# Optimization experiments

Hardware: AMD Instinct MI355X
Metric: run time of the kernel (lower is better)

Reference implementation:

```python
import jax, jax.numpy as jnp
import numpy as np

N_NODES = 100000
N_EDGES = 1600000
DIM = 128
N_LAYERS = 3   # num_gc_layers
N_RES = 3      # residual VQ layers
N_CODE = 16    # codebook_size
N_GRAPHS = 512
BN_EPS = 1e-5
COMMIT_W = 0.25


def _l2norm(v):
    return v * jax.lax.rsqrt(jnp.sum(v * v, axis=-1, keepdims=True) + 1e-12)


def setup_inputs() -> dict:
    key = jax.random.key(0)
    ks = jax.random.split(key, 8)
    s = 0.05
    x = jax.random.normal(ks[0], (N_NODES, DIM), jnp.float32)
    edge_index = jax.random.randint(ks[1], (2, N_EDGES), 0, N_NODES)
    batch = jnp.sort(jax.random.randint(ks[2], (N_NODES,), 0, N_GRAPHS))
    W1 = jax.random.normal(ks[3], (N_LAYERS, DIM, DIM), jnp.float32) * s
    b1 = jnp.zeros((N_LAYERS, DIM), jnp.float32)
    W2 = jax.random.normal(ks[4], (N_LAYERS, DIM, DIM), jnp.float32) * s
    b2 = jnp.zeros((N_LAYERS, DIM), jnp.float32)
    gamma = jnp.ones((N_LAYERS, DIM), jnp.float32)
    beta = jnp.zeros((N_LAYERS, DIM), jnp.float32)
    codebooks = jax.random.normal(ks[5], (N_LAYERS, N_RES, N_CODE, DIM), jnp.float32)
    return dict(x=x, edge_index=edge_index, batch=batch, W1=W1, b1=b1,
                W2=W2, b2=b2, gamma=gamma, beta=beta, codebooks=codebooks)


def reference(x, edge_index, batch, W1, b1, W2, b2, gamma, beta, codebooks):
    src, dst = edge_index[0], edge_index[1]
    h = x
    xs, ids = [], []
    commit_loss = jnp.float32(0.0)
    for i in range(N_LAYERS):
        # GINConv, eps=0: MLP((1+eps)*x + sum_{j->i} x_j)
        agg = jax.ops.segment_sum(h[src], dst, num_segments=N_NODES)
        h = agg + h
        h = jax.nn.relu(h @ W1[i] + b1[i]) @ W2[i] + b2[i]  # Linear-ReLU-Linear
        h = jax.nn.relu(h)                                   # outer F.relu
        # BatchNorm1d (training-mode batch stats, biased variance)
        mean = jnp.mean(h, axis=0)
        var = jnp.var(h, axis=0)
        h = (h - mean) * jax.lax.rsqrt(var + BN_EPS) * gamma[i] + beta[i]
        xs.append(h)
        # Residual VQ with cosine-sim codebook (3 residual layers)
        r = h
        lids = []
        for l in range(N_RES):
            cbn = _l2norm(codebooks[i, l])           # [K, D] normalized codebook
            sim = _l2norm(r) @ cbn.T                  # [N, K] cosine similarity
            idx = jnp.argmax(sim, axis=-1)            # nearest code
            q = cbn[idx]                              # quantized residual
            commit_loss = commit_loss + COMMIT_W * jnp.mean(
                (jax.lax.stop_gradient(q) - r) ** 2)
            r = r - jax.lax.stop_gradient(q)
            lids.append(idx)
        ids.append(jnp.stack(lids, axis=1))           # [N, N_RES]
    xs_cat = jnp.concatenate(xs, axis=1)              # [N, DIM*N_LAYERS]
    xpool = jax.ops.segment_sum(xs_cat, batch, num_segments=N_GRAPHS)
    id_cat = jnp.concatenate(ids, axis=1)             # [N, N_RES*N_LAYERS]
    return xpool, xs_cat, commit_loss, id_cat
```

## Files before the change

### kernel.cpp

```cpp
#include <hip/hip_runtime.h>
#include <hip/hip_bf16.h>

#define N_NODES 100000
#define N_EDGES 1600000
#define DIM 128
#define NLAY 3
#define NRES 3
#define NCODE 16
#define NGRAPH 512
#define SCAN_NB ((N_NODES + 255) / 256)
#define GEMM_NB ((N_NODES + 63) / 64)

using bf16 = __hip_bfloat16;

__device__ inline void atomAddD(double* p, double v) { unsafeAtomicAdd(p, v); }

__device__ inline double ldx(const void* p, long i, int isbf) {
  if (isbf) return (double)__bfloat162float(((const bf16*)p)[i]);
  return (double)((const float*)p)[i];
}
__device__ inline void stout(void* p, long i, double v, int isbf) {
  if (isbf) ((bf16*)p)[i] = __float2bfloat16((float)v);
  else ((float*)p)[i] = (float)v;
}

__global__ void k_detect(const unsigned int* __restrict__ x, int* __restrict__ flag) {
  int tid = threadIdx.x;
  int cnt = 0;
  for (int j = tid; j < 1024; j += 256) {
    unsigned int u = x[j];
    int e = (u >> 7) & 0xFF;
    cnt += (e >= 100 && e <= 135) ? 1 : 0;
  }
  __shared__ int sh[256];
  sh[tid] = cnt; __syncthreads();
  for (int s = 128; s; s >>= 1) { if (tid < s) sh[tid] += sh[tid + s]; __syncthreads(); }
  if (tid == 0) flag[0] = (sh[0] > 512) ? 1 : 0;
}

__global__ __launch_bounds__(256) void k_convert_f(const void* __restrict__ x, float* __restrict__ hf,
                                                   long n, const int* __restrict__ flag) {
  int isbf = flag[0];
  long i = (long)blockIdx.x * 256 + threadIdx.x;
  if (i < n) hf[i] = (float)ldx(x, i, isbf);
}

__global__ __launch_bounds__(256) void k_hist(const int* __restrict__ ei, int* __restrict__ deg) {
  int e = blockIdx.x * 256 + threadIdx.x;
  if (e < N_EDGES) atomicAdd(&deg[ei[N_EDGES + e]], 1);
}

__global__ __launch_bounds__(256) void k_scan1(const int* __restrict__ deg, int* __restrict__ bsum) {
  int i = blockIdx.x * 256 + threadIdx.x;
  int v = (i < N_NODES) ? deg[i] : 0;
  for (int o = 32; o; o >>= 1) v += __shfl_xor(v, o);
  __shared__ int sh[4];
  if ((threadIdx.x & 63) == 0) sh[threadIdx.x >> 6] = v;
  __syncthreads();
  if (threadIdx.x == 0) bsum[blockIdx.x] = sh[0] + sh[1] + sh[2] + sh[3];
}

__global__ void k_scan2(int* __restrict__ bsum) {
  __shared__ int sh[512];
  int t = threadIdx.x;
  int v = (t < SCAN_NB) ? bsum[t] : 0;
  sh[t] = v; __syncthreads();
  for (int s = 1; s < 512; s <<= 1) {
    int add = (t >= s) ? sh[t - s] : 0;
    __syncthreads();
    sh[t] += add;
    __syncthreads();
  }
  if (t < SCAN_NB) bsum[t] = sh[t] - v;
}

__global__ __launch_bounds__(256) void k_scan3(const int* __restrict__ deg, const int* __restrict__ bsum,
                                               int* __restrict__ ofs, int* __restrict__ cursor) {
  int t = threadIdx.x;
  int i = blockIdx.x * 256 + t;
  int v = (i < N_NODES) ? deg[i] : 0;
  __shared__ int sh[256];
  sh[t] = v; __syncthreads();
  for (int s = 1; s < 256; s <<= 1) {
    int add = (t >= s) ? sh[t - s] : 0;
    __syncthreads();
    sh[t] += add;
    __syncthreads();
  }
  int excl = sh[t] - v + bsum[blockIdx.x];
  if (i < N_NODES) { ofs[i] = excl; cursor[i] = excl; }
  if (i == N_NODES - 1) ofs[N_NODES] = excl + v;
}

__global__ __launch_bounds__(256) void k_fill(const int* __restrict__ ei, int* __restrict__ cursor,
                                              int* __restrict__ csr) {
  int e = blockIdx.x * 256 + threadIdx.x;
  if (e < N_EDGES) {
    int d = ei[N_EDGES + e];
    int p = atomicAdd(&cursor[d], 1);
    csr[p] = ei[e];
  }
}

__global__ void k_cbn(const void* __restrict__ cb, double* __restrict__ cbn, const int* __restrict__ flag) {
  int isbf = flag[0];
  int b = blockIdx.x, d = threadIdx.x;
  double v0 = ldx(cb, (long)b * DIM + d, isbf);
  double v1 = ldx(cb, (long)b * DIM + d + 64, isbf);
  double ss = v0 * v0 + v1 * v1;
  for (int o = 32; o; o >>= 1) ss += __shfl_xor(ss, o);
  double inv = 1.0 / sqrt(ss + 1e-12);
  cbn[b * DIM + d] = v0 * inv;
  cbn[b * DIM + d + 64] = v1 * inv;
}

__global__ void k_gram(const double* __restrict__ cbn, double* __restrict__ G) {
  int b = blockIdx.x, t = threadIdx.x;
  int l = b / (48 * 48); int rem = b % (48 * 48); int a = rem / 48, c = rem % 48;
  const double* ra = cbn + (long)(l * 48 + a) * DIM;
  const double* rc = cbn + (long)(l * 48 + c) * DIM;
  double s = ra[t] * rc[t] + ra[t + 64] * rc[t + 64];
  for (int o = 32; o; o >>= 1) s += __shfl_xor(s, o);
  if (t == 0) G[b] = s;
}

__global__ __launch_bounds__(256) void k_gathgemm1(const float* __restrict__ hf,
                                                   const int* __restrict__ ofs,
                                                   const int* __restrict__ csr,
                                                   const float* __restrict__ W,
                                                   const float* __restrict__ bias,
                                                   float* __restrict__ out) {
  __shared__ float ul[64 * DIM];
  int tid = threadIdx.x;
  long base = (long)blockIdx.x * 64;
  int wave = tid >> 6, lane = tid & 63;
  for (int i = 0; i < 16; i++) {
    int row = wave * 16 + i;
    long node = base + row;
    double accx = 0.0, accy = 0.0;
    if (node < N_NODES) {
      int beg = ofs[node], end = ofs[node + 1];
      float2 sv = *(const float2*)&hf[node * DIM + lane * 2];
      accx = (double)sv.x; accy = (double)sv.y;
      int j = beg;
      for (; j + 7 < end; j += 8) {
        int s0 = csr[j], s1 = csr[j + 1], s2 = csr[j + 2], s3 = csr[j + 3];
        int s4 = csr[j + 4], s5 = csr[j + 5], s6 = csr[j + 6], s7 = csr[j + 7];
        float2 v0 = *(const float2*)&hf[(long)s0 * DIM + lane * 2];
        float2 v1 = *(const float2*)&hf[(long)s1 * DIM + lane * 2];
        float2 v2 = *(const float2*)&hf[(long)s2 * DIM + lane * 2];
        float2 v3 = *(const float2*)&hf[(long)s3 * DIM + lane * 2];
        float2 v4 = *(const float2*)&hf[(long)s4 * DIM + lane * 2];
        float2 v5 = *(const float2*)&hf[(long)s5 * DIM + lane * 2];
        float2 v6 = *(const float2*)&hf[(long)s6 * DIM + lane * 2];
        float2 v7 = *(const float2*)&hf[(long)s7 * DIM + lane * 2];
        accx += (double)v0.x; accy += (double)v0.y;
        accx += (double)v1.x; accy += (double)v1.y;
        accx += (double)v2.x; accy += (double)v2.y;
        accx += (double)v3.x; accy += (double)v3.y;
        accx += (double)v4.x; accy += (double)v4.y;
        accx += (double)v5.x; accy += (double)v5.y;
        accx += (double)v6.x; accy += (double)v6.y;
        accx += (double)v7.x; accy += (double)v7.y;
      }
      for (; j < end; j++) {
        int s0 = csr[j];
        float2 v0 = *(const float2*)&hf[(long)s0 * DIM + lane * 2];
        accx += (double)v0.x; accy += (double)v0.y;
      }
    }
    *(float2*)&ul[row * DIM + lane * 2] = make_float2((float)accx, (float)accy);
  }
  __syncthreads();
  int cl = tid & 31;
  int rw = tid >> 5;
  int c0 = cl * 4;
  float acc[8][4] = {};
  for (int k = 0; k < DIM; k += 4) {
    float4 w0 = *(const float4*)&W[(k + 0) * DIM + c0];
    float4 w1 = *(const float4*)&W[(k + 1) * DIM + c0];
    float4 w2 = *(const float4*)&W[(k + 2) * DIM + c0];
    float4 w3 = *(const float4*)&W[(k + 3) * DIM + c0];
#pragma unroll
    for (int r = 0; r < 8; r++) {
      float4 u = *(const float4*)&ul[(rw * 8 + r) * DIM + k];
      acc[r][0] += u.x * w0.x + u.y * w1.x + u.z * w2.x + u.w * w3.x;
      acc[r][1] += u.x * w0.y + u.y * w1.y + u.z * w2.y + u.w * w3.y;
      acc[r][2] += u.x * w0.z + u.y * w1.z + u.z * w2.z + u.w * w3.z;
      acc[r][3] += u.x * w0.w + u.y * w1.w + u.z * w2.w + u.w * w3.w;
    }
  }
  float4 bv = *(const float4*)&bias[c0];
#pragma unroll
  for (int r = 0; r < 8; r++) {
    long row = base + rw * 8 + r;
    if (row < N_NODES) {
      float4 o;
      o.x = fmaxf(acc[r][0] + bv.x, 0.f);
      o.y = fmaxf(acc[r][1] + bv.y, 0.f);
      o.z = fmaxf(acc[r][2] + bv.z, 0.f);
      o.w = fmaxf(acc[r][3] + bv.w, 0.f);
      *(float4*)&out[row * DIM + c0] = o;
    }
  }
}

__global__ __launch_bounds__(256) void k_gemm_relu_f(const float* __restrict__ in,
                                                     const float* __restrict__ W,
                                                     const float* __restrict__ bias,
                                                     float* __restrict__ out) {
  __shared__ float ul[64 * DIM];
  int tid = threadIdx.x;
  long base = (long)blockIdx.x * 64;
  for (int j = tid; j < 64 * DIM / 4; j += 256) {
    long row = base + (j >> 5);
    float4 v = make_float4(0.f, 0.f, 0.f, 0.f);
    if (row < N_NODES) v = *(const float4*)&in[base * DIM + (long)j * 4];
    *(float4*)&ul[j * 4] = v;
  }
  __syncthreads();
  int cl = tid & 31;
  int rw = tid >> 5;
  int c0 = cl * 4;
  float acc[8][4] = {};
  for (int k = 0; k < DIM; k += 4) {
    float4 w0 = *(const float4*)&W[(k + 0) * DIM + c0];
    float4 w1 = *(const float4*)&W[(k + 1) * DIM + c0];
    float4 w2 = *(const float4*)&W[(k + 2) * DIM + c0];
    float4 w3 = *(const float4*)&W[(k + 3) * DIM + c0];
#pragma unroll
    for (int r = 0; r < 8; r++) {
      float4 u = *(const float4*)&ul[(rw * 8 + r) * DIM + k];
      acc[r][0] += u.x * w0.x + u.y * w1.x + u.z * w2.x + u.w * w3.x;
      acc[r][1] += u.x * w0.y + u.y * w1.y + u.z * w2.y + u.w * w3.y;
      acc[r][2] += u.x * w0.z + u.y * w1.z + u.z * w2.z + u.w * w3.z;
      acc[r][3] += u.x * w0.w + u.y * w1.w + u.z * w2.w + u.w * w3.w;
    }
  }
  float4 bv = *(const float4*)&bias[c0];
#pragma unroll
  for (int r = 0; r < 8; r++) {
    long row = base + rw * 8 + r;
    if (row < N_NODES) {
      float4 o;
      o.x = fmaxf(acc[r][0] + bv.x, 0.f);
      o.y = fmaxf(acc[r][1] + bv.y, 0.f);
      o.z = fmaxf(acc[r][2] + bv.z, 0.f);
      o.w = fmaxf(acc[r][3] + bv.w, 0.f);
      *(float4*)&out[row * DIM + c0] = o;
    }
  }
}

__global__ __launch_bounds__(256) void k_bn_stats(const float* __restrict__ h, double* __restrict__ stats) {
  int tid = threadIdx.x; int col = tid & 127; int half = tid >> 7;
  double s = 0.0, s2 = 0.0;
  for (long r = blockIdx.x * 2 + half; r < N_NODES; r += 2048) {
    double v = (double)h[r * DIM + col];
    s += v; s2 += v * v;
  }
  __shared__ double ls[256], ls2[256];
  ls[tid] = s; ls2[tid] = s2;
  __syncthreads();
  if (tid < 128) {
    atomAddD(&stats[col], ls[tid] + ls[tid + 128]);
    atomAddD(&stats[DIM + col], ls2[tid] + ls2[tid + 128]);
  }
}

__global__ void k_bn_prep(const double* __restrict__ stats, const void* __restrict__ gamma,
                          const void* __restrict__ beta, double* __restrict__ ss,
                          int l, const int* __restrict__ flag) {
  int isbf = flag[0];
  int d = threadIdx.x;
  double mean = stats[d] / (double)N_NODES;
  double var = stats[DIM + d] / (double)N_NODES - mean * mean;
  double sc = ldx(gamma, (long)l * DIM + d, isbf) / sqrt(var + 1e-5);
  ss[d] = sc;
  ss[DIM + d] = ldx(beta, (long)l * DIM + d, isbf) - mean * sc;
}

__global__ __launch_bounds__(256) void k_post(float* __restrict__ h,
                                              const double* __restrict__ ss,
                                              const int* __restrict__ batch,
                                              void* __restrict__ out,
                                              double* __restrict__ xpool,
                                              double* __restrict__ hh,
                                              int l, const int* __restrict__ flag) {
  __shared__ float hl[64 * 132];
  __shared__ double hq[64 * 4];
  __shared__ int sbat[64];
  int isbf = flag[0];
  int tid = threadIdx.x;
  long base = (long)blockIdx.x * 64;
  if (tid < 64) {
    long row = base + tid;
    sbat[tid] = (row < N_NODES) ? batch[row] : -1;
  }
  int d = tid & 127, half = tid >> 7;
  double sc = ss[d], sh = ss[DIM + d];
  const long XS_BASE = (long)NGRAPH * DIM * NLAY;
  for (int rr = half; rr < 64; rr += 2) {
    long row = base + rr;
    float vf = 0.f;
    if (row < N_NODES) {
      double v = (double)h[row * DIM + d] * sc + sh;
      vf = (float)v;
      h[row * DIM + d] = vf;
      stout(out, XS_BASE + row * (DIM * NLAY) + l * DIM + d, v, isbf);
    }
    hl[rr * 132 + d] = vf;
  }
  __syncthreads();
  {
    int row = tid >> 2, q = tid & 3;
    double s2 = 0.0;
    const float* hp = &hl[row * 132 + q * 32];
#pragma unroll
    for (int i = 0; i < 32; i++) { double v = (double)hp[i]; s2 += v * v; }
    hq[row * 4 + q] = s2;
  }
  __syncthreads();
  if (tid < 64) {
    long n = base + tid;
    if (n < N_NODES) hh[n] = hq[tid * 4] + hq[tid * 4 + 1] + hq[tid * 4 + 2] + hq[tid * 4 + 3];
  } else if (tid >= 128) {
    int dd = tid - 128;
    int g = sbat[0];
    double acc = 0.0;
    for (int r = 0; r < 64; r++) {
      int gg = sbat[r];
      if (gg < 0) break;
      if (gg != g) {
        atomAddD(&xpool[(long)g * (DIM * NLAY) + l * DIM + dd], acc);
        acc = 0.0; g = gg;
      }
      acc += (double)hl[r * 132 + dd];
    }
    atomAddD(&xpool[(long)g * (DIM * NLAY) + l * DIM + dd], acc);
  }
}

__global__ __launch_bounds__(256) void k_dotH(const float* __restrict__ hn,
                                              const double* __restrict__ cbnL,
                                              float* __restrict__ dH) {
  __shared__ double cl[48 * 134];
  int tid = threadIdx.x;
  for (int j = tid; j < 48 * DIM; j += 256) { int c = j >> 7, k = j & 127; cl[c * 134 + k] = cbnL[j]; }
  __syncthreads();
  int ct = tid & 7; int c0 = ct * 6; int rt = tid >> 3;
  long r0 = (long)blockIdx.x * 64 + rt; long r1 = r0 + 32;
  long r0c = r0 < N_NODES ? r0 : (N_NODES - 1);
  long r1c = r1 < N_NODES ? r1 : (N_NODES - 1);
  double acc0[6] = {}, acc1[6] = {};
  for (int k = 0; k < DIM; k += 4) {
    float4 h0 = *(const float4*)&hn[r0c * DIM + k];
    float4 h1 = *(const float4*)&hn[r1c * DIM + k];
#pragma unroll
    for (int j = 0; j < 6; j++) {
      double2 ca = *(const double2*)&cl[(c0 + j) * 134 + k];
      double2 cb = *(const double2*)&cl[(c0 + j) * 134 + k + 2];
      acc0[j] += (double)h0.x * ca.x + (double)h0.y * ca.y + (double)h0.z * cb.x + (double)h0.w * cb.y;
      acc1[j] += (double)h1.x * ca.x + (double)h1.y * ca.y + (double)h1.z * cb.x + (double)h1.w * cb.y;
    }
  }
  if (r0 < N_NODES) {
#pragma unroll
    for (int j = 0; j < 6; j++) dH[r0 * 48 + c0 + j] = (float)acc0[j];
  }
  if (r1 < N_NODES) {
#pragma unroll
    for (int j = 0; j < 6; j++) dH[r1 * 48 + c0 + j] = (float)acc1[j];
  }
}

__global__ __launch_bounds__(256) void k_vq(const float* __restrict__ dH, const double* __restrict__ hh,
                                            const double* __restrict__ G, void* __restrict__ out,
                                            double* __restrict__ commit, int l, const int* __restrict__ flag) {
  int isbf = flag[0];
  __shared__ double Gl[48 * 48];
  int tid = threadIdx.x;
  for (int j = tid; j < 48 * 48; j += 256) Gl[j] = G[j];
  __syncthreads();
  long n = (long)blockIdx.x * 256 + tid;
  double csum = 0.0;
  if (n < N_NODES) {
    double dh[48];
#pragma unroll
    for (int c = 0; c < 48; c++) dh[c] = (double)dH[n * 48 + c];
    int i0 = 0; double b0 = dh[0];
#pragma unroll
    for (int c = 1; c < 16; c++) { if (dh[c] > b0) { b0 = dh[c]; i0 = c; } }
    int i1 = 0; double b1 = dh[16] - Gl[i0 * 48 + 16];
#pragma unroll
    for (int c = 1; c < 16; c++) {
      double s = dh[16 + c] - Gl[i0 * 48 + 16 + c];
      if (s > b1) { b1 = s; i1 = c; }
    }
    int i2 = 0; double b2 = dh[32] - Gl[i0 * 48 + 32] - Gl[(16 + i1) * 48 + 32];
#pragma unroll
    for (int c = 1; c < 16; c++) {
      double s = dh[32 + c] - Gl[i0 * 48 + 32 + c] - Gl[(16 + i1) * 48 + 32 + c];
      if (s > b2) { b2 = s; i2 = c; }
    }
    double r1s = hh[n] - 2.0 * b0 + Gl[i0 * 48 + i0];
    double r2s = r1s - 2.0 * b1 + Gl[(16 + i1) * 48 + 16 + i1];
    double r3s = r2s - 2.0 * b2 + Gl[(32 + i2) * 48 + 32 + i2];
    csum = r1s + r2s + r3s;
    const long IDS_BASE = (long)NGRAPH * DIM * NLAY + (long)N_NODES * DIM * NLAY + 1;
    long base = IDS_BASE + n * (NLAY * NRES) + l * NRES;
    stout(out, base + 0, (double)i0, isbf);
    stout(out, base + 1, (double)i1, isbf);
    stout(out, base + 2, (double)i2, isbf);
  }
  for (int o = 32; o; o >>= 1) csum += __shfl_xor(csum, o);
  if ((tid & 63) == 0 && csum != 0.0) atomAddD(commit, csum);
}

__global__ __launch_bounds__(256) void k_out(const double* __restrict__ xpool, const double* __restrict__ commit,
                                             void* __restrict__ out, const int* __restrict__ flag) {
  int isbf = flag[0];
  long i = (long)blockIdx.x * 256 + threadIdx.x;
  const long NP = (long)NGRAPH * DIM * NLAY;
  if (i < NP) {
    stout(out, i, xpool[i], isbf);
  } else if (i == NP) {
    double c = commit[0] * (0.25 / ((double)N_NODES * (double)DIM));
    stout(out, NP + (long)N_NODES * DIM * NLAY, c, isbf);
  }
}

extern "C" void kernel_launch(void* const* d_in, const int* in_sizes, int n_in,
                              void* d_out, int out_size, void* d_ws, size_t ws_size,
                              hipStream_t stream) {
  const void* x = d_in[0];
  const int* ei = (const int*)d_in[1];
  const int* batch = (const int*)d_in[2];
  const void* W1 = d_in[3];
  const void* b1 = d_in[4];
  const void* W2 = d_in[5];
  const void* b2 = d_in[6];
  const void* gamma = d_in[7];
  const void* beta = d_in[8];
  const void* cb = d_in[9];

  double* w = (double*)d_ws;
  double* cbn = w;
  double* G = cbn + 18432;
  double* stats = G + 6912;
  double* ss = stats + 256;
  double* hh = ss + 256;
  double* xpool = hh + N_NODES;
  double* commit = xpool + (long)NGRAPH * DIM * NLAY;
  float* W1f = (float*)(commit + 2);
  float* W2f = W1f + 49152;
  float* b1f = W2f + 49152;
  float* b2f = b1f + 384;
  float* H  = b2f + 384;
  float* T1 = H + 12800000;
  float* T2 = T1 + 12800000;
  float* dH = T2 + 12800000;
  int* ibuf = (int*)(dH + 4800000);
  int* flag = ibuf;
  int* deg = ibuf + 64;
  int* ofs = deg + N_NODES;
  int* cursor = ofs + N_NODES + 1;
  int* csr = cursor + N_NODES;
  int* bsum = csr + N_EDGES;

  k_detect<<<1, 256, 0, stream>>>((const unsigned int*)x, flag);
  hipMemsetAsync(xpool, 0, ((long)NGRAPH * DIM * NLAY + 1) * sizeof(double), stream);
  hipMemsetAsync(deg, 0, N_NODES * sizeof(int), stream);
  k_convert_f<<<50000, 256, 0, stream>>>(x, H, (long)N_NODES * DIM, flag);
  k_convert_f<<<192, 256, 0, stream>>>(W1, W1f, 49152, flag);
  k_convert_f<<<192, 256, 0, stream>>>(W2, W2f, 49152, flag);
  k_convert_f<<<2, 256, 0, stream>>>(b1, b1f, 384, flag);
  k_convert_f<<<2, 256, 0, stream>>>(b2, b2f, 384, flag);
  k_cbn<<<NLAY * NRES * NCODE, 64, 0, stream>>>(cb, cbn, flag);
  k_gram<<<NLAY * 48 * 48, 64, 0, stream>>>(cbn, G);
  k_hist<<<(N_EDGES + 255) / 256, 256, 0, stream>>>(ei, deg);
  k_scan1<<<SCAN_NB, 256, 0, stream>>>(deg, bsum);
  k_scan2<<<1, 512, 0, stream>>>(bsum);
  k_scan3<<<SCAN_NB, 256, 0, stream>>>(deg, bsum, ofs, cursor);
  k_fill<<<(N_EDGES + 255) / 256, 256, 0, stream>>>(ei, cursor, csr);

  for (int l = 0; l < NLAY; l++) {
    k_gathgemm1<<<GEMM_NB, 256, 0, stream>>>(H, ofs, csr, W1f + l * DIM * DIM, b1f + l * DIM, T2);
    k_gemm_relu_f<<<GEMM_NB, 256, 0, stream>>>(T2, W2f + l * DIM * DIM, b2f + l * DIM, T1);
    hipMemsetAsync(stats, 0, 256 * sizeof(double), stream);
    k_bn_stats<<<1024, 256, 0, stream>>>(T1, stats);
    k_bn_prep<<<1, 128, 0, stream>>>(stats, gamma, beta, ss, l, flag);
    k_post<<<GEMM_NB, 256, 0, stream>>>(T1, ss, batch, d_out, xpool, hh, l, flag);
    k_dotH<<<1563, 256, 0, stream>>>(T1, cbn + (long)l * 48 * DIM, dH);
    k_vq<<<391, 256, 0, stream>>>(dH, hh, G + l * 48 * 48, d_out, commit, l, flag);
    float* t = H; H = T1; T1 = t;
  }
  k_out<<<769, 256, 0, stream>>>(xpool, commit, d_out, flag);
}
```

Measured before the change: 1.711 ms.

## Split gather from GEMM, fuse BN stats into second GEMM and prep into post

The fused gather+GEMM kernel is split into a standalone gather kernel that runs one wave per node across many more blocks, followed by the plain GEMM. This raises parallelism for the latency-bound irregular gather. Batch-norm column sums are now accumulated in the epilogue of the second GEMM, with atomics spread over 8 slabs to reduce contention. The separate stats pass over T1 and the bn_prep launch are removed, and k_post derives scale and shift itself. In exchange the aggregated features take an extra round trip through global memory.

```diff
diff --git a/kernel.cpp b/kernel.cpp
--- a/kernel.cpp
+++ b/kernel.cpp
@@ -102,6 +102,35 @@
   }
 }
 
+__global__ __launch_bounds__(256) void k_gather(const float* __restrict__ hf,
+                                                const int* __restrict__ ofs,
+                                                const int* __restrict__ csr,
+                                                float* __restrict__ outQ) {
+  int node = blockIdx.x * 4 + (threadIdx.x >> 6);
+  int lane = threadIdx.x & 63;
+  int beg = ofs[node], end = ofs[node + 1];
+  float2 sv = *(const float2*)&hf[(long)node * DIM + lane * 2];
+  double accx = (double)sv.x, accy = (double)sv.y;
+  int j = beg;
+  for (; j + 3 < end; j += 4) {
+    int s0 = csr[j], s1 = csr[j + 1], s2 = csr[j + 2], s3 = csr[j + 3];
+    float2 v0 = *(const float2*)&hf[(long)s0 * DIM + lane * 2];
+    float2 v1 = *(const float2*)&hf[(long)s1 * DIM + lane * 2];
+    float2 v2 = *(const float2*)&hf[(long)s2 * DIM + lane * 2];
+    float2 v3 = *(const float2*)&hf[(long)s3 * DIM + lane * 2];
+    accx += (double)v0.x; accy += (double)v0.y;
+    accx += (double)v1.x; accy += (double)v1.y;
+    accx += (double)v2.x; accy += (double)v2.y;
+    accx += (double)v3.x; accy += (double)v3.y;
+  }
+  for (; j < end; j++) {
+    int s0 = csr[j];
+    float2 v0 = *(const float2*)&hf[(long)s0 * DIM + lane * 2];
+    accx += (double)v0.x; accy += (double)v0.y;
+  }
+  *(float2*)&outQ[(long)node * DIM + lane * 2] = make_float2((float)accx, (float)accy);
+}
+
 __global__ void k_cbn(const void* __restrict__ cb, double* __restrict__ cbn, const int* __restrict__ flag) {
   int isbf = flag[0];
   int b = blockIdx.x, d = threadIdx.x;
@@ -122,87 +151,6 @@
   double s = ra[t] * rc[t] + ra[t + 64] * rc[t + 64];
   for (int o = 32; o; o >>= 1) s += __shfl_xor(s, o);
   if (t == 0) G[b] = s;
-}
-
-__global__ __launch_bounds__(256) void k_gathgemm1(const float* __restrict__ hf,
-                                                   const int* __restrict__ ofs,
-                                                   const int* __restrict__ csr,
-                                                   const float* __restrict__ W,
-                                                   const float* __restrict__ bias,
-                                                   float* __restrict__ out) {
-  __shared__ float ul[64 * DIM];
-  int tid = threadIdx.x;
-  long base = (long)blockIdx.x * 64;
-  int wave = tid >> 6, lane = tid & 63;
-  for (int i = 0; i < 16; i++) {
-    int row = wave * 16 + i;
-    long node = base + row;
-    double accx = 0.0, accy = 0.0;
-    if (node < N_NODES) {
-      int beg = ofs[node], end = ofs[node + 1];
-      float2 sv = *(const float2*)&hf[node * DIM + lane * 2];
-      accx = (double)sv.x; accy = (double)sv.y;
-      int j = beg;
-      for (; j + 7 < end; j += 8) {
-        int s0 = csr[j], s1 = csr[j + 1], s2 = csr[j + 2], s3 = csr[j + 3];
-        int s4 = csr[j + 4], s5 = csr[j + 5], s6 = csr[j + 6], s7 = csr[j + 7];
-        float2 v0 = *(const float2*)&hf[(long)s0 * DIM + lane * 2];
-        float2 v1 = *(const float2*)&hf[(long)s1 * DIM + lane * 2];
-        float2 v2 = *(const float2*)&hf[(long)s2 * DIM + lane * 2];
-        float2 v3 = *(const float2*)&hf[(long)s3 * DIM + lane * 2];
-        float2 v4 = *(const float2*)&hf[(long)s4 * DIM + lane * 2];
-        float2 v5 = *(const float2*)&hf[(long)s5 * DIM + lane * 2];
-        float2 v6 = *(const float2*)&hf[(long)s6 * DIM + lane * 2];
-        float2 v7 = *(const float2*)&hf[(long)s7 * DIM + lane * 2];
-        accx += (double)v0.x; accy += (double)v0.y;
-        accx += (double)v1.x; accy += (double)v1.y;
-        accx += (double)v2.x; accy += (double)v2.y;
-        accx += (double)v3.x; accy += (double)v3.y;
-        accx += (double)v4.x; accy += (double)v4.y;
-        accx += (double)v5.x; accy += (double)v5.y;
-        accx += (double)v6.x; accy += (double)v6.y;
-        accx += (double)v7.x; accy += (double)v7.y;
-      }
-      for (; j < end; j++) {
-        int s0 = csr[j];
-        float2 v0 = *(const float2*)&hf[(long)s0 * DIM + lane * 2];
-        accx += (double)v0.x; accy += (double)v0.y;
-      }
-    }
-    *(float2*)&ul[row * DIM + lane * 2] = make_float2((float)accx, (float)accy);
-  }
-  __syncthreads();
-  int cl = tid & 31;
-  int rw = tid >> 5;
-  int c0 = cl * 4;
-  float acc[8][4] = {};
-  for (int k = 0; k < DIM; k += 4) {
-    float4 w0 = *(const float4*)&W[(k + 0) * DIM + c0];
-    float4 w1 = *(const float4*)&W[(k + 1) * DIM + c0];
-    float4 w2 = *(const float4*)&W[(k + 2) * DIM + c0];
-    float4 w3 = *(const float4*)&W[(k + 3) * DIM + c0];
-#pragma unroll
-    for (int r = 0; r < 8; r++) {
-      float4 u = *(const float4*)&ul[(rw * 8 + r) * DIM + k];
-      acc[r][0] += u.x * w0.x + u.y * w1.x + u.z * w2.x + u.w * w3.x;
-      acc[r][1] += u.x * w0.y + u.y * w1.y + u.z * w2.y + u.w * w3.y;
-      acc[r][2] += u.x * w0.z + u.y * w1.z + u.z * w2.z + u.w * w3.z;
-      acc[r][3] += u.x * w0.w + u.y * w1.w + u.z * w2.w + u.w * w3.w;
-    }
-  }
-  float4 bv = *(const float4*)&bias[c0];
-#pragma unroll
-  for (int r = 0; r < 8; r++) {
-    long row = base + rw * 8 + r;
-    if (row < N_NODES) {
-      float4 o;
-      o.x = fmaxf(acc[r][0] + bv.x, 0.f);
-      o.y = fmaxf(acc[r][1] + bv.y, 0.f);
-      o.z = fmaxf(acc[r][2] + bv.z, 0.f);
-      o.w = fmaxf(acc[r][3] + bv.w, 0.f);
-      *(float4*)&out[row * DIM + c0] = o;
-    }
-  }
 }
 
 __global__ __launch_bounds__(256) void k_gemm_relu_f(const float* __restrict__ in,
@@ -252,36 +200,80 @@
   }
 }
 
-__global__ __launch_bounds__(256) void k_bn_stats(const float* __restrict__ h, double* __restrict__ stats) {
-  int tid = threadIdx.x; int col = tid & 127; int half = tid >> 7;
-  double s = 0.0, s2 = 0.0;
-  for (long r = blockIdx.x * 2 + half; r < N_NODES; r += 2048) {
-    double v = (double)h[r * DIM + col];
-    s += v; s2 += v * v;
-  }
-  __shared__ double ls[256], ls2[256];
-  ls[tid] = s; ls2[tid] = s2;
+__global__ __launch_bounds__(256) void k_gemm_relu_stats(const float* __restrict__ in,
+                                                         const float* __restrict__ W,
+                                                         const float* __restrict__ bias,
+                                                         float* __restrict__ out,
+                                                         double* __restrict__ stats8) {
+  __shared__ __align__(16) float ul[64 * DIM];
+  int tid = threadIdx.x;
+  long base = (long)blockIdx.x * 64;
+  for (int j = tid; j < 64 * DIM / 4; j += 256) {
+    long row = base + (j >> 5);
+    float4 v = make_float4(0.f, 0.f, 0.f, 0.f);
+    if (row < N_NODES) v = *(const float4*)&in[base * DIM + (long)j * 4];
+    *(float4*)&ul[j * 4] = v;
+  }
+  __syncthreads();
+  int cl = tid & 31;
+  int rw = tid >> 5;
+  int c0 = cl * 4;
+  float acc[8][4] = {};
+  for (int k = 0; k < DIM; k += 4) {
+    float4 w0 = *(const float4*)&W[(k + 0) * DIM + c0];
+    float4 w1 = *(const float4*)&W[(k + 1) * DIM + c0];
+    float4 w2 = *(const float4*)&W[(k + 2) * DIM + c0];
+    float4 w3 = *(const float4*)&W[(k + 3) * DIM + c0];
+#pragma unroll
+    for (int r = 0; r < 8; r++) {
+      float4 u = *(const float4*)&ul[(rw * 8 + r) * DIM + k];
+      acc[r][0] += u.x * w0.x + u.y * w1.x + u.z * w2.x + u.w * w3.x;
+      acc[r][1] += u.x * w0.y + u.y * w1.y + u.z * w2.y + u.w * w3.y;
+      acc[r][2] += u.x * w0.z + u.y * w1.z + u.z * w2.z + u.w * w3.z;
+      acc[r][3] += u.x * w0.w + u.y * w1.w + u.z * w2.w + u.w * w3.w;
+    }
+  }
+  float4 bv = *(const float4*)&bias[c0];
+  double cs0 = 0.0, cs1 = 0.0, cs2 = 0.0, cs3 = 0.0;
+  double q0 = 0.0, q1 = 0.0, q2 = 0.0, q3 = 0.0;
+#pragma unroll
+  for (int r = 0; r < 8; r++) {
+    long row = base + rw * 8 + r;
+    if (row < N_NODES) {
+      float4 o;
+      o.x = fmaxf(acc[r][0] + bv.x, 0.f);
+      o.y = fmaxf(acc[r][1] + bv.y, 0.f);
+      o.z = fmaxf(acc[r][2] + bv.z, 0.f);
+      o.w = fmaxf(acc[r][3] + bv.w, 0.f);
+      *(float4*)&out[row * DIM + c0] = o;
+      double dx = (double)o.x, dy = (double)o.y, dz = (double)o.z, dw = (double)o.w;
+      cs0 += dx; q0 += dx * dx;
+      cs1 += dy; q1 += dy * dy;
+      cs2 += dz; q2 += dz * dz;
+      cs3 += dw; q3 += dw * dw;
+    }
+  }
+  __syncthreads();
+  double* sred = (double*)ul;
+  sred[rw * 128 + c0 + 0] = cs0; sred[1024 + rw * 128 + c0 + 0] = q0;
+  sred[rw * 128 + c0 + 1] = cs1; sred[1024 + rw * 128 + c0 + 1] = q1;
+  sred[rw * 128 + c0 + 2] = cs2; sred[1024 + rw * 128 + c0 + 2] = q2;
+  sred[rw * 128 + c0 + 3] = cs3; sred[1024 + rw * 128 + c0 + 3] = q3;
   __syncthreads();
   if (tid < 128) {
-    atomAddD(&stats[col], ls[tid] + ls[tid + 128]);
-    atomAddD(&stats[DIM + col], ls2[tid] + ls2[tid + 128]);
-  }
-}
-
-__global__ void k_bn_prep(const double* __restrict__ stats, const void* __restrict__ gamma,
-                          const void* __restrict__ beta, double* __restrict__ ss,
-                          int l, const int* __restrict__ flag) {
-  int isbf = flag[0];
-  int d = threadIdx.x;
-  double mean = stats[d] / (double)N_NODES;
-  double var = stats[DIM + d] / (double)N_NODES - mean * mean;
-  double sc = ldx(gamma, (long)l * DIM + d, isbf) / sqrt(var + 1e-5);
-  ss[d] = sc;
-  ss[DIM + d] = ldx(beta, (long)l * DIM + d, isbf) - mean * sc;
+    double S = 0.0, S2 = 0.0;
+#pragma unroll
+    for (int i = 0; i < 8; i++) { S += sred[i * 128 + tid]; S2 += sred[1024 + i * 128 + tid]; }
+    int slab = blockIdx.x & 7;
+    atomAddD(&stats8[slab * 256 + tid], S);
+    atomAddD(&stats8[slab * 256 + 128 + tid], S2);
+  }
 }
 
 __global__ __launch_bounds__(256) void k_post(float* __restrict__ h,
-                                              const double* __restrict__ ss,
+                                              const double* __restrict__ stats8,
+                                              const void* __restrict__ gamma,
+                                              const void* __restrict__ beta,
                                               const int* __restrict__ batch,
                                               void* __restrict__ out,
                                               double* __restrict__ xpool,
@@ -289,16 +281,28 @@
                                               int l, const int* __restrict__ flag) {
   __shared__ float hl[64 * 132];
   __shared__ double hq[64 * 4];
+  __shared__ double ssl[256];
   __shared__ int sbat[64];
   int isbf = flag[0];
   int tid = threadIdx.x;
   long base = (long)blockIdx.x * 64;
+  if (tid < 128) {
+    double sum = 0.0, sumsq = 0.0;
+#pragma unroll
+    for (int s8 = 0; s8 < 8; s8++) { sum += stats8[s8 * 256 + tid]; sumsq += stats8[s8 * 256 + 128 + tid]; }
+    double mean = sum / (double)N_NODES;
+    double var = sumsq / (double)N_NODES - mean * mean;
+    double sc = ldx(gamma, (long)l * DIM + tid, isbf) / sqrt(var + 1e-5);
+    ssl[tid] = sc;
+    ssl[DIM + tid] = ldx(beta, (long)l * DIM + tid, isbf) - mean * sc;
+  }
   if (tid < 64) {
     long row = base + tid;
     sbat[tid] = (row < N_NODES) ? batch[row] : -1;
   }
+  __syncthreads();
   int d = tid & 127, half = tid >> 7;
-  double sc = ss[d], sh = ss[DIM + d];
+  double sc = ssl[d], sh = ssl[DIM + d];
   const long XS_BASE = (long)NGRAPH * DIM * NLAY;
   for (int rr = half; rr < 64; rr += 2) {
     long row = base + rr;
@@ -447,9 +451,8 @@
   double* w = (double*)d_ws;
   double* cbn = w;
   double* G = cbn + 18432;
-  double* stats = G + 6912;
-  double* ss = stats + 256;
-  double* hh = ss + 256;
+  double* stats8 = G + 6912;
+  double* hh = stats8 + 2048;
   double* xpool = hh + N_NODES;
   double* commit = xpool + (long)NGRAPH * DIM * NLAY;
   float* W1f = (float*)(commit + 2);
@@ -485,12 +488,11 @@
   k_fill<<<(N_EDGES + 255) / 256, 256, 0, stream>>>(ei, cursor, csr);
 
   for (int l = 0; l < NLAY; l++) {
-    k_gathgemm1<<<GEMM_NB, 256, 0, stream>>>(H, ofs, csr, W1f + l * DIM * DIM, b1f + l * DIM, T2);
-    k_gemm_relu_f<<<GEMM_NB, 256, 0, stream>>>(T2, W2f + l * DIM * DIM, b2f + l * DIM, T1);
-    hipMemsetAsync(stats, 0, 256 * sizeof(double), stream);
-    k_bn_stats<<<1024, 256, 0, stream>>>(T1, stats);
-    k_bn_prep<<<1, 128, 0, stream>>>(stats, gamma, beta, ss, l, flag);
-    k_post<<<GEMM_NB, 256, 0, stream>>>(T1, ss, batch, d_out, xpool, hh, l, flag);
+    k_gather<<<N_NODES / 4, 256, 0, stream>>>(H, ofs, csr, T1);
+    k_gemm_relu_f<<<GEMM_NB, 256, 0, stream>>>(T1, W1f + l * DIM * DIM, b1f + l * DIM, T2);
+    hipMemsetAsync(stats8, 0, 2048 * sizeof(double), stream);
+    k_gemm_relu_stats<<<GEMM_NB, 256, 0, stream>>>(T2, W2f + l * DIM * DIM, b2f + l * DIM, T1, stats8);
+    k_post<<<GEMM_NB, 256, 0, stream>>>(T1, stats8, gamma, beta, batch, d_out, xpool, hh, l, flag);
     k_dotH<<<1563, 256, 0, stream>>>(T1, cbn + (long)l * 48 * DIM, dH);
     k_vq<<<391, 256, 0, stream>>>(dH, hh, G + l * 48 * 48, d_out, commit, l, flag);
     float* t = H; H = T1; T1 = t;
```

Result: faster. 1.597 ms (-6.7%).
